# Performance work log

Measured on AMD Instinct MI355X. Metric: run time of the kernel, lower is better.

The kernel has to match this reference:

```python
import jax, jax.numpy as jnp
import numpy as np

EPS = 1e-12  # torch F.normalize eps


def _l2norm(x, axis):
    return x / jnp.maximum(jnp.linalg.norm(x, axis=axis, keepdims=True), EPS)


def setup_inputs() -> dict:
    key = jax.random.key(0)
    ks = jax.random.split(key, 8)
    B, N, D_in, H, K, D_out = 16, 1024, 1024, 512, 64, 1024
    return {
        "input_data": jax.random.normal(ks[0], (B, N, D_in), dtype=jnp.float32),
        "fc1_w": jax.random.normal(ks[1], (H, D_in), dtype=jnp.float32) * 0.02,
        "fc1_b": jax.random.normal(ks[2], (H,), dtype=jnp.float32) * 0.02,
        "conv_w": jax.random.normal(ks[3], (K, H), dtype=jnp.float32) * 0.1,
        "conv_b": jax.random.normal(ks[4], (K,), dtype=jnp.float32) * 0.1,
        "centroids": jax.random.normal(ks[5], (K, H), dtype=jnp.float32),
        "fc2_w": jax.random.normal(ks[6], (D_out, K * H), dtype=jnp.float32) * 0.01,
        "fc2_b": jax.random.normal(ks[7], (D_out,), dtype=jnp.float32) * 0.01,
    }


def reference(input_data, fc1_w, fc1_b, conv_w, conv_b, centroids, fc2_w, fc2_b):
    # fc1 + relu: [B, N, H]
    h = jax.nn.relu(jnp.einsum('bnd,hd->bnh', input_data, fc1_w) + fc1_b)
    # NetVLAD input layout: [B, H, N] (the (N,1) spatial dims collapse to N)
    x = jnp.swapaxes(h, 1, 2)
    # normalize descriptors across feature dim (F.normalize(x, p=2, dim=1))
    xn = _l2norm(x, axis=1)
    # 1x1-conv soft assignment -> softmax over clusters: [B, K, N]
    logits = jnp.einsum('kh,bhn->bkn', conv_w, xn) + conv_b[None, :, None]
    a = jax.nn.softmax(logits, axis=1)
    # vlad_{bkh} = sum_n a_{bkn} (xn_{bhn} - c_{kh})  (fused, no [B,K,H,N] tensor)
    vlad = jnp.einsum('bkn,bhn->bkh', a, xn) - a.sum(axis=-1)[:, :, None] * centroids[None]
    vlad = _l2norm(vlad, axis=2)              # intra-normalization
    vlad = vlad.reshape(vlad.shape[0], -1)    # [B, K*H]
    vlad = _l2norm(vlad, axis=1)              # global L2 norm
    # fc2 + relu: [B, out_dim]
    return jax.nn.relu(vlad @ fc2_w.T + fc2_b)
```

## Files before the change

### kernel.cpp

```cpp
#include <hip/hip_runtime.h>
#include <hip/hip_bf16.h>

typedef __bf16  bf16x8 __attribute__((ext_vector_type(8)));
typedef float   f32x4  __attribute__((ext_vector_type(4)));

#define DEV __device__ __forceinline__

DEV ushort f2b(float f){
  union { float f; unsigned u; } c; c.f = f;
  unsigned u = c.u;
  unsigned r = (u + 0x7FFFu + ((u >> 16) & 1u)) >> 16;
  return (ushort)r;
}
DEV float b2f(ushort h){
  union { unsigned u; float f; } c; c.u = ((unsigned)h) << 16;
  return c.f;
}
DEV void gload_lds16(const void* g, void* l){
  __builtin_amdgcn_global_load_lds(
      (const __attribute__((address_space(1))) void*)g,
      (__attribute__((address_space(3))) void*)l,
      16, 0, 0);
}
DEV bf16x8 cvt8(float4 a0, float4 a1){
  bf16x8 t;
  t[0]=(__bf16)a0.x; t[1]=(__bf16)a0.y; t[2]=(__bf16)a0.z; t[3]=(__bf16)a0.w;
  t[4]=(__bf16)a1.x; t[5]=(__bf16)a1.y; t[6]=(__bf16)a1.z; t[7]=(__bf16)a1.w;
  return t;
}

__global__ void prep(const float* __restrict__ W1, const float* __restrict__ CW,
                     const float* __restrict__ CB,
                     ushort* __restrict__ W1b, ushort* __restrict__ CWb,
                     float* __restrict__ CBp){
  int bid = blockIdx.x, tid = threadIdx.x;
  if(bid < 512){
    int i = bid * 256 + tid;
    float4 f = ((const float4*)W1)[i];
    ushort4 o; o.x = f2b(f.x); o.y = f2b(f.y); o.z = f2b(f.z); o.w = f2b(f.w);
    ((ushort4*)W1b)[i] = o;
  } else if(bid < 768){
    int i = (bid - 512) * 256 + tid;
    int r = i >> 9;
    CWb[i] = (r < 64) ? f2b(CW[i]) : (ushort)0;
  } else {
    if(tid < 128) CBp[tid] = (tid < 64) ? CB[tid] : 0.0f;
  }
}

__global__ __launch_bounds__(512) void fc1n(
    const float* __restrict__ A, const ushort* __restrict__ B,
    const float* __restrict__ bias, ushort* __restrict__ XN,
    ushort* __restrict__ XNT)
{
  const int K = 1024;
  __shared__ __align__(16) char smem[81920];
  __shared__ float ssq_p[4][64];
  __shared__ float scale_s[64];
  const int tid = threadIdx.x, lane = tid & 63, wid = tid >> 6;
  const int bm0 = blockIdx.x * 64;
  const int wr = (wid >> 2) * 32;
  const int wc = (wid & 3) * 128;
  const int wcol = wid & 3;

  const int srow = tid >> 3;
  const int sseg = tid & 7;
  const char* asrc = (const char*)A + (size_t)(bm0 + srow) * 4096
                     + (sseg ^ (srow & 7)) * 16;
  const int bslot = (tid & 3) ^ ((tid >> 3) & 3);
  const ushort* bg = B + (size_t)(tid >> 2) * K + bslot * 8;

  f32x4 acc[2][8];
  #pragma unroll
  for(int i = 0; i < 2; i++)
    #pragma unroll
    for(int j = 0; j < 8; j++) acc[i][j] = (f32x4){0.f, 0.f, 0.f, 0.f};

  const int arow = lane & 15;
  const int khalf = lane >> 4;

#define STAGE_F1N(buf, kb) do { \
    gload_lds16(asrc + (kb), smem + (buf) * 8192 + tid * 16); \
    const ushort* bs_ = bg + ((kb) >> 2); \
    char* bd_ = smem + 16384 + (buf) * 32768 + tid * 16; \
    gload_lds16(bs_,           bd_); \
    gload_lds16(bs_ + 128 * K, bd_ + 8192); \
    gload_lds16(bs_ + 256 * K, bd_ + 16384); \
    gload_lds16(bs_ + 384 * K, bd_ + 24576); \
  } while(0)

  STAGE_F1N(0, 0);
  __syncthreads();

  int cur = 0;
  for(int ks = 0; ks < 32; ++ks){
    if(ks + 1 < 32) STAGE_F1N(cur ^ 1, (ks + 1) * 128);
    bf16x8 af[2], bfr[8];
    #pragma unroll
    for(int mi = 0; mi < 2; mi++){
      int r = wr + mi * 16 + arow;
      const char* base = smem + cur * 8192 + r * 128;
      float4 a0 = *(const float4*)(base + (((khalf * 2)     ^ (r & 7)) * 16));
      float4 a1 = *(const float4*)(base + (((khalf * 2 + 1) ^ (r & 7)) * 16));
      af[mi] = cvt8(a0, a1);
    }
    #pragma unroll
    for(int ni = 0; ni < 8; ni++){
      int r = wc + ni * 16 + arow;
      bfr[ni] = *(const bf16x8*)(smem + 16384 + cur * 32768
                                 + r * 64 + ((khalf ^ ((r >> 1) & 3)) * 16));
    }
    #pragma unroll
    for(int mi = 0; mi < 2; mi++)
      #pragma unroll
      for(int ni = 0; ni < 8; ni++)
        acc[mi][ni] = __builtin_amdgcn_mfma_f32_16x16x32_bf16(af[mi], bfr[ni], acc[mi][ni], 0, 0, 0);
    __syncthreads();
    cur ^= 1;
  }
#undef STAGE_F1N

  float bv[8];
  #pragma unroll
  for(int ni = 0; ni < 8; ni++) bv[ni] = bias[wc + ni * 16 + (lane & 15)];
  float p[2][4];
  #pragma unroll
  for(int mi = 0; mi < 2; mi++)
    #pragma unroll
    for(int i = 0; i < 4; i++){
      float s = 0.f;
      #pragma unroll
      for(int ni = 0; ni < 8; ni++){
        float v = fmaxf(acc[mi][ni][i] + bv[ni], 0.f);
        acc[mi][ni][i] = v;
        s += v * v;
      }
      p[mi][i] = s;
    }
  #pragma unroll
  for(int o = 1; o < 16; o <<= 1)
    #pragma unroll
    for(int mi = 0; mi < 2; mi++)
      #pragma unroll
      for(int i = 0; i < 4; i++)
        p[mi][i] += __shfl_xor(p[mi][i], o, 64);
  if((lane & 15) == 0){
    int g = lane >> 4;
    #pragma unroll
    for(int mi = 0; mi < 2; mi++)
      #pragma unroll
      for(int i = 0; i < 4; i++)
        ssq_p[wcol][wr + mi * 16 + g * 4 + i] = p[mi][i];
  }
  __syncthreads();
  if(tid < 64){
    float s = ssq_p[0][tid] + ssq_p[1][tid] + ssq_p[2][tid] + ssq_p[3][tid];
    scale_s[tid] = 1.0f / fmaxf(sqrtf(s), 1e-12f);
  }
  __syncthreads();

  ushort* Tb = (ushort*)smem;
  #pragma unroll
  for(int mi = 0; mi < 2; mi++)
    #pragma unroll
    for(int i = 0; i < 4; i++){
      int rt = wr + mi * 16 + (lane >> 4) * 4 + i;
      float sc = scale_s[rt];
      #pragma unroll
      for(int ni = 0; ni < 8; ni++){
        int h = wc + ni * 16 + (lane & 15);
        ushort v = f2b(acc[mi][ni][i] * sc);
        XN[(size_t)(bm0 + rt) * 512 + h] = v;
        Tb[h * 66 + rt] = v;
      }
    }
  __syncthreads();
  {
    const int bb = bm0 >> 10, n0b = bm0 & 1023;
    const char* tb = (const char*)smem + tid * 132;
    unsigned tmp[32];
    #pragma unroll
    for(int j = 0; j < 32; j++) tmp[j] = *(const unsigned*)(tb + j * 4);
    ushort* dst = XNT + ((size_t)bb * 512 + tid) * 1024 + n0b;
    #pragma unroll
    for(int u = 0; u < 8; u++){
      uint4 w; w.x = tmp[u*4]; w.y = tmp[u*4+1]; w.z = tmp[u*4+2]; w.w = tmp[u*4+3];
      *(uint4*)(dst + u * 8) = w;
    }
  }
}

__global__ __launch_bounds__(256) void gemm_lgsm(
    const ushort* __restrict__ A, const ushort* __restrict__ B,
    const float* __restrict__ bias,
    ushort* __restrict__ AThi, ushort* __restrict__ ATlo)
{
  const int K = 512;
  __shared__ __align__(16) ushort As[2][64 * 32];
  __shared__ __align__(16) ushort Bs[2][128 * 32];
  __shared__ float as_[64][65];
  const int tid  = threadIdx.x;
  const int lane = tid & 63, wid = tid >> 6;
  const int bm0 = blockIdx.x * 64;
  const int wr = (wid >> 1) * 32, wc = (wid & 1) * 64;

  const int slot = (tid & 3) ^ ((tid >> 3) & 3);
  const ushort* ag = A + (size_t)(bm0 + (tid >> 2)) * K + slot * 8;
  const ushort* bg = B + (size_t)(tid >> 2) * K + slot * 8;

  f32x4 acc[2][4];
  #pragma unroll
  for(int i = 0; i < 2; i++)
    #pragma unroll
    for(int j = 0; j < 4; j++) acc[i][j] = (f32x4){0.f, 0.f, 0.f, 0.f};

  const int arow = lane & 15;
  const int khalf = lane >> 4;

  gload_lds16(ag,          &As[0][tid * 8]);
  gload_lds16(bg,          &Bs[0][tid * 8]);
  gload_lds16(bg + 64 * K, &Bs[0][2048 + tid * 8]);
  __syncthreads();

  int cur = 0;
  for(int ks = 0; ks < 16; ++ks){
    if(ks + 1 < 16){
      const ushort* agn = ag + (ks + 1) * 32;
      const ushort* bgn = bg + (ks + 1) * 32;
      gload_lds16(agn,          &As[cur ^ 1][tid * 8]);
      gload_lds16(bgn,          &Bs[cur ^ 1][tid * 8]);
      gload_lds16(bgn + 64 * K, &Bs[cur ^ 1][2048 + tid * 8]);
    }
    bf16x8 af[2], bfr[4];
    #pragma unroll
    for(int mi = 0; mi < 2; mi++){
      int r = wr + mi * 16 + arow;
      af[mi] = *(const bf16x8*)&As[cur][r * 32 + ((khalf ^ ((r >> 1) & 3)) * 8)];
    }
    #pragma unroll
    for(int ni = 0; ni < 4; ni++){
      int r = wc + ni * 16 + arow;
      bfr[ni] = *(const bf16x8*)&Bs[cur][r * 32 + ((khalf ^ ((r >> 1) & 3)) * 8)];
    }
    #pragma unroll
    for(int mi = 0; mi < 2; mi++)
      #pragma unroll
      for(int ni = 0; ni < 4; ni++)
        acc[mi][ni] = __builtin_amdgcn_mfma_f32_16x16x32_bf16(af[mi], bfr[ni], acc[mi][ni], 0, 0, 0);
    __syncthreads();
    cur ^= 1;
  }

  if((wid & 1) == 0){
    #pragma unroll
    for(int ni = 0; ni < 4; ni++){
      float bvv = bias[ni * 16 + (lane & 15)];
      #pragma unroll
      for(int mi = 0; mi < 2; mi++)
        #pragma unroll
        for(int i = 0; i < 4; i++) acc[mi][ni][i] += bvv;
    }
    #pragma unroll
    for(int mi = 0; mi < 2; mi++)
      #pragma unroll
      for(int i = 0; i < 4; i++){
        int row = wr + mi * 16 + (lane >> 4) * 4 + i;
        float m = fmaxf(fmaxf(acc[mi][0][i], acc[mi][1][i]),
                        fmaxf(acc[mi][2][i], acc[mi][3][i]));
        #pragma unroll
        for(int o = 1; o < 16; o <<= 1) m = fmaxf(m, __shfl_xor(m, o, 64));
        float e[4], s = 0.f;
        #pragma unroll
        for(int ni = 0; ni < 4; ni++){ e[ni] = __expf(acc[mi][ni][i] - m); s += e[ni]; }
        #pragma unroll
        for(int o = 1; o < 16; o <<= 1) s += __shfl_xor(s, o, 64);
        float inv = 1.0f / s;
        #pragma unroll
        for(int ni = 0; ni < 4; ni++)
          as_[row][ni * 16 + (lane & 15)] = e[ni] * inv;
      }
  }
  __syncthreads();

  const int b = bm0 >> 10, n0 = bm0 & 1023;
  const int nl = tid & 63, kq = tid >> 6;
  #pragma unroll
  for(int q = 0; q < 16; q++){
    int k = kq * 16 + q;
    float a = as_[nl][k];
    ushort hi = f2b(a);
    float lo = a - b2f(hi);
    size_t idx = ((size_t)b * 64 + k) * 1024 + n0 + nl;
    AThi[idx] = hi;
    ATlo[idx] = f2b(lo);
  }
}

__global__ __launch_bounds__(512) void vlad_mfma(
    const ushort* __restrict__ AThi, const ushort* __restrict__ ATlo,
    const ushort* __restrict__ XNT, const float* __restrict__ cent,
    ushort* __restrict__ vlb, float* __restrict__ ssq)
{
  __shared__ __align__(16) ushort Ah[2][16 * 32];
  __shared__ __align__(16) ushort Al[2][16 * 32];
  __shared__ __align__(16) ushort Xs[2][512 * 32];
  __shared__ float red[8][16];
  __shared__ float scale_s[16], ssqn_s[16];
  const int tid = threadIdx.x, lane = tid & 63, wid = tid >> 6;
  const int b = blockIdx.x, kg = blockIdx.y;
  const int k0 = kg * 16;
  const int hw = wid;
  const int arow = lane & 15, khalf = lane >> 4;

  const int xslot = (tid & 3) ^ ((tid >> 3) & 3);
  const ushort* xg = XNT + ((size_t)b * 512 + (tid >> 2)) * 1024 + xslot * 8;
  const int aslot = (lane & 3) ^ ((lane >> 3) & 3);
  const ushort* ahg = AThi + ((size_t)b * 64 + k0 + (lane >> 2)) * 1024 + aslot * 8;
  const ushort* alg = ATlo + ((size_t)b * 64 + k0 + (lane >> 2)) * 1024 + aslot * 8;

  f32x4 acc[4];
  #pragma unroll
  for(int i = 0; i < 4; i++) acc[i] = (f32x4){0.f, 0.f, 0.f, 0.f};
  f32x4 asum = (f32x4){0.f, 0.f, 0.f, 0.f};
  bf16x8 ones;
  #pragma unroll
  for(int j = 0; j < 8; j++) ones[j] = (__bf16)1.0f;

#define STAGE_VL(buf, n0v) do { \
    char* xd = (char*)&Xs[buf][0] + tid * 16; \
    gload_lds16(xg + (n0v),                xd); \
    gload_lds16(xg + (n0v) + 128 * 1024,   xd + 8192); \
    gload_lds16(xg + (n0v) + 256 * 1024,   xd + 16384); \
    gload_lds16(xg + (n0v) + 384 * 1024,   xd + 24576); \
    if(wid == 0)      gload_lds16(ahg + (n0v), (char*)&Ah[buf][0] + lane * 16); \
    else if(wid == 1) gload_lds16(alg + (n0v), (char*)&Al[buf][0] + lane * 16); \
  } while(0)

  STAGE_VL(0, 0);
  __syncthreads();

  int cur = 0;
  for(int ks = 0; ks < 32; ++ks){
    if(ks + 1 < 32) STAGE_VL(cur ^ 1, (ks + 1) * 32);
    bf16x8 ah, al, bfr[4];
    {
      int sl = khalf ^ ((arow >> 1) & 3);
      ah = *(const bf16x8*)&Ah[cur][arow * 32 + sl * 8];
      al = *(const bf16x8*)&Al[cur][arow * 32 + sl * 8];
    }
    #pragma unroll
    for(int ni = 0; ni < 4; ni++){
      int r = hw * 64 + ni * 16 + arow;
      bfr[ni] = *(const bf16x8*)&Xs[cur][r * 32 + ((khalf ^ ((r >> 1) & 3)) * 8)];
    }
    asum = __builtin_amdgcn_mfma_f32_16x16x32_bf16(ah, ones, asum, 0, 0, 0);
    asum = __builtin_amdgcn_mfma_f32_16x16x32_bf16(al, ones, asum, 0, 0, 0);
    #pragma unroll
    for(int ni = 0; ni < 4; ni++){
      acc[ni] = __builtin_amdgcn_mfma_f32_16x16x32_bf16(ah, bfr[ni], acc[ni], 0, 0, 0);
      acc[ni] = __builtin_amdgcn_mfma_f32_16x16x32_bf16(al, bfr[ni], acc[ni], 0, 0, 0);
    }
    __syncthreads();
    cur ^= 1;
  }
#undef STAGE_VL

  float vl[4][4];
  #pragma unroll
  for(int ni = 0; ni < 4; ni++)
    #pragma unroll
    for(int i = 0; i < 4; i++){
      int r_ = (lane >> 4) * 4 + i;
      int h = hw * 64 + ni * 16 + (lane & 15);
      vl[ni][i] = acc[ni][i] - asum[i] * cent[(size_t)(k0 + r_) * 512 + h];
    }
  float sq[4];
  #pragma unroll
  for(int i = 0; i < 4; i++){
    float s = 0.f;
    #pragma unroll
    for(int ni = 0; ni < 4; ni++) s += vl[ni][i] * vl[ni][i];
    sq[i] = s;
  }
  #pragma unroll
  for(int o = 1; o < 16; o <<= 1)
    #pragma unroll
    for(int i = 0; i < 4; i++) sq[i] += __shfl_xor(sq[i], o, 64);
  if((lane & 15) == 0){
    #pragma unroll
    for(int i = 0; i < 4; i++) red[hw][(lane >> 4) * 4 + i] = sq[i];
  }
  __syncthreads();
  if(tid < 16){
    float s = 0.f;
    #pragma unroll
    for(int w = 0; w < 8; w++) s += red[w][tid];
    float sc = 1.0f / fmaxf(sqrtf(s), 1e-12f);
    scale_s[tid] = sc;
    ssqn_s[tid] = s * sc * sc;
  }
  __syncthreads();
  if(tid < 4)
    ssq[b * 16 + kg * 4 + tid] = ssqn_s[tid * 4] + ssqn_s[tid * 4 + 1]
                               + ssqn_s[tid * 4 + 2] + ssqn_s[tid * 4 + 3];
  #pragma unroll
  for(int ni = 0; ni < 4; ni++)
    #pragma unroll
    for(int i = 0; i < 4; i++){
      int r_ = (lane >> 4) * 4 + i;
      int h = hw * 64 + ni * 16 + (lane & 15);
      vlb[(size_t)b * 32768 + (size_t)(k0 + r_) * 512 + h] = f2b(vl[ni][i] * scale_s[r_]);
    }
}

__global__ __launch_bounds__(256) void fc2_mfma(const float* __restrict__ W,
                                                const ushort* __restrict__ vlb,
                                                float* __restrict__ part){
  __shared__ __align__(16) float Bs[2][128 * 32];
  const int tid = threadIdx.x, lane = tid & 63, wid = tid >> 6;
  const int c0 = blockIdx.x * 128;
  const int kc = blockIdx.y;
  const size_t kbase = (size_t)kc * 256;

  const int srow = tid >> 3;
  const int seg  = tid & 7;
  f32x4 acc0 = (f32x4){0.f,0.f,0.f,0.f};
  f32x4 acc1 = (f32x4){0.f,0.f,0.f,0.f};

  const int arow = lane & 15;
  const int khalf = lane >> 4;
  const int cRow0 = wid * 32 + (lane & 15);
  const int cRow1 = cRow0 + 16;

  #pragma unroll
  for(int pass = 0; pass < 4; ++pass){
    int row = pass * 32 + srow;
    const char* src = (const char*)W + (size_t)(c0 + row) * 131072
                      + kbase * 4 + ((seg ^ (row & 7)) * 16);
    gload_lds16(src, (char*)&Bs[0][0] + row * 128 + seg * 16);
  }
  __syncthreads();

  int cur = 0;
  for(int ks = 0; ks < 8; ++ks){
    if(ks + 1 < 8){
      #pragma unroll
      for(int pass = 0; pass < 4; ++pass){
        int row = pass * 32 + srow;
        const char* src = (const char*)W + (size_t)(c0 + row) * 131072
                          + (kbase + (ks + 1) * 32) * 4 + ((seg ^ (row & 7)) * 16);
        gload_lds16(src, (char*)&Bs[cur ^ 1][0] + row * 128 + seg * 16);
      }
    }
    bf16x8 af = *(const bf16x8*)((const char*)vlb + (size_t)arow * 65536
                                 + (kbase + ks * 32 + khalf * 8) * 2);
    int t0 = khalf * 2;
    const char* bsc = (const char*)&Bs[cur][0];
    float4 b00 = *(const float4*)(bsc + cRow0 * 128 + ((t0     ^ (cRow0 & 7)) * 16));
    float4 b01 = *(const float4*)(bsc + cRow0 * 128 + (((t0+1) ^ (cRow0 & 7)) * 16));
    float4 b10 = *(const float4*)(bsc + cRow1 * 128 + ((t0     ^ (cRow1 & 7)) * 16));
    float4 b11 = *(const float4*)(bsc + cRow1 * 128 + (((t0+1) ^ (cRow1 & 7)) * 16));
    bf16x8 bf0 = cvt8(b00, b01);
    bf16x8 bf1 = cvt8(b10, b11);

    acc0 = __builtin_amdgcn_mfma_f32_16x16x32_bf16(af, bf0, acc0, 0, 0, 0);
    acc1 = __builtin_amdgcn_mfma_f32_16x16x32_bf16(af, bf1, acc1, 0, 0, 0);
    __syncthreads();
    cur ^= 1;
  }

  #pragma unroll
  for(int i = 0; i < 4; ++i){
    int b = (lane >> 4) * 4 + i;
    int d0 = c0 + wid * 32 + (lane & 15);
    part[((size_t)kc * 16 + b) * 1024 + d0]      = acc0[i];
    part[((size_t)kc * 16 + b) * 1024 + d0 + 16] = acc1[i];
  }
}

__global__ __launch_bounds__(256) void fin(const float* __restrict__ part, const float* __restrict__ ssq,
                                           const float* __restrict__ b2, float* __restrict__ out){
  __shared__ float red[4][64];
  int lane = threadIdx.x & 63, wq = threadIdx.x >> 6;
  int o = blockIdx.x * 64 + lane;
  int b = o >> 10, d = o & 1023;
  float s = 0;
  #pragma unroll
  for(int i = 0; i < 32; i++){
    int t = wq * 32 + i;
    s += part[((size_t)t * 16 + b) * 1024 + d];
  }
  red[wq][lane] = s;
  __syncthreads();
  if(wq == 0){
    float g = 0;
    #pragma unroll
    for(int kg = 0; kg < 16; kg++) g += ssq[b * 16 + kg];
    float gsv = 1.0f / fmaxf(sqrtf(g), 1e-12f);
    float tot = red[0][lane] + red[1][lane] + red[2][lane] + red[3][lane];
    out[o] = fmaxf(gsv * tot + b2[d], 0.0f);
  }
}

extern "C" void kernel_launch(void* const* d_in, const int* in_sizes, int n_in,
                              void* d_out, int out_size, void* d_ws, size_t ws_size,
                              hipStream_t stream){
  const float* X    = (const float*)d_in[0];
  const float* W1   = (const float*)d_in[1];
  const float* B1   = (const float*)d_in[2];
  const float* CW   = (const float*)d_in[3];
  const float* CB   = (const float*)d_in[4];
  const float* CENT = (const float*)d_in[5];
  const float* W2   = (const float*)d_in[6];
  const float* B2   = (const float*)d_in[7];
  float* out = (float*)d_out;
  char* ws = (char*)d_ws;

  ushort* W1b  = (ushort*)(ws + 0);
  ushort* CWb  = (ushort*)(ws + 1048576);
  float*  CBp  = (float*) (ws + 1179648);
  ushort* XN   = (ushort*)(ws + 1180160);
  ushort* XNT  = (ushort*)(ws + 17957376);
  ushort* AThi = (ushort*)(ws + 34734592);
  ushort* ATlo = (ushort*)(ws + 36831744);
  ushort* VLb  = (ushort*)(ws + 38928896);
  float*  SSQ  = (float*) (ws + 39977472);
  float*  PART = (float*) (ws + 39978496);

  prep<<<769, 256, 0, stream>>>(W1, CW, CB, W1b, CWb, CBp);
  fc1n<<<256, 512, 0, stream>>>(X, W1b, B1, XN, XNT);
  gemm_lgsm<<<256, 256, 0, stream>>>(XN, CWb, CBp, AThi, ATlo);
  vlad_mfma<<<dim3(16, 4), 512, 0, stream>>>(AThi, ATlo, XNT, CENT, VLb, SSQ);
  fc2_mfma<<<dim3(8, 128), 256, 0, stream>>>(W2, VLb, PART);
  fin<<<256, 256, 0, stream>>>(PART, SSQ, B2, out);
}
```

Measured before the change: 118.6 us.

## Fuse soft-assignment GEMM and softmax into fc1 normalize kernel

Folds the conv/soft-assignment GEMM and softmax into the fc1 kernel, keeping the normalized 64x512 tile in shared memory instead of writing the XN buffer and reading it back in a separate launch. The conv weights are pre-swizzled in prep and streamed into LDS per block. This removes one kernel launch and a 16 MB global round trip. In exchange, LDS per block grows to about 150 KB, which limits residency to one block per CU and adds serial work at the end of fc1.

After: 110.5 us. -6.9%, faster.

```diff
diff --git a/kernel.cpp b/kernel.cpp
--- a/kernel.cpp
+++ b/kernel.cpp
@@ -15,6 +15,16 @@
 DEV float b2f(ushort h){
   union { unsigned u; float f; } c; c.u = ((unsigned)h) << 16;
   return c.f;
+}
+DEV float wredsum(float v){
+  #pragma unroll
+  for(int o = 32; o > 0; o >>= 1) v += __shfl_xor(v, o, 64);
+  return v;
+}
+DEV float wredmax(float v){
+  #pragma unroll
+  for(int o = 32; o > 0; o >>= 1) v = fmaxf(v, __shfl_xor(v, o, 64));
+  return v;
 }
 DEV void gload_lds16(const void* g, void* l){
   __builtin_amdgcn_global_load_lds(
@@ -39,22 +49,24 @@
     float4 f = ((const float4*)W1)[i];
     ushort4 o; o.x = f2b(f.x); o.y = f2b(f.y); o.z = f2b(f.z); o.w = f2b(f.w);
     ((ushort4*)W1b)[i] = o;
-  } else if(bid < 768){
+  } else if(bid < 640){
     int i = (bid - 512) * 256 + tid;
-    int r = i >> 9;
-    CWb[i] = (r < 64) ? f2b(CW[i]) : (ushort)0;
+    int k = i >> 9, h = i & 511;
+    int seg = h >> 3, pos = h & 7;
+    CWb[(k << 9) + ((seg ^ (k & 7)) << 3) + pos] = f2b(CW[i]);
   } else {
     if(tid < 128) CBp[tid] = (tid < 64) ? CB[tid] : 0.0f;
   }
 }
 
-__global__ __launch_bounds__(512) void fc1n(
+__global__ __launch_bounds__(512) void fc1sm(
     const float* __restrict__ A, const ushort* __restrict__ B,
-    const float* __restrict__ bias, ushort* __restrict__ XN,
-    ushort* __restrict__ XNT)
+    const float* __restrict__ bias, const ushort* __restrict__ CWb,
+    const float* __restrict__ CBp, ushort* __restrict__ XNT,
+    ushort* __restrict__ AThi, ushort* __restrict__ ATlo)
 {
   const int K = 1024;
-  __shared__ __align__(16) char smem[81920];
+  __shared__ __align__(16) char smem[149504];
   __shared__ float ssq_p[4][64];
   __shared__ float scale_s[64];
   const int tid = threadIdx.x, lane = tid & 63, wid = tid >> 6;
@@ -159,7 +171,8 @@
   }
   __syncthreads();
 
-  ushort* Tb = (ushort*)smem;
+  ushort* Tb  = (ushort*)(smem + 81920);
+  ushort* xnm = (ushort*)smem;
   #pragma unroll
   for(int mi = 0; mi < 2; mi++)
     #pragma unroll
@@ -170,14 +183,15 @@
       for(int ni = 0; ni < 8; ni++){
         int h = wc + ni * 16 + (lane & 15);
         ushort v = f2b(acc[mi][ni][i] * sc);
-        XN[(size_t)(bm0 + rt) * 512 + h] = v;
         Tb[h * 66 + rt] = v;
+        xnm[rt * 520 + h] = v;
       }
     }
   __syncthreads();
+
+  const int bb = bm0 >> 10, n0b = bm0 & 1023;
   {
-    const int bb = bm0 >> 10, n0b = bm0 & 1023;
-    const char* tb = (const char*)smem + tid * 132;
+    const char* tb = (const char*)smem + 81920 + tid * 132;
     unsigned tmp[32];
     #pragma unroll
     for(int j = 0; j < 32; j++) tmp[j] = *(const unsigned*)(tb + j * 4);
@@ -188,111 +202,61 @@
       *(uint4*)(dst + u * 8) = w;
     }
   }
-}
-
-__global__ __launch_bounds__(256) void gemm_lgsm(
-    const ushort* __restrict__ A, const ushort* __restrict__ B,
-    const float* __restrict__ bias,
-    ushort* __restrict__ AThi, ushort* __restrict__ ATlo)
-{
-  const int K = 512;
-  __shared__ __align__(16) ushort As[2][64 * 32];
-  __shared__ __align__(16) ushort Bs[2][128 * 32];
-  __shared__ float as_[64][65];
-  const int tid  = threadIdx.x;
-  const int lane = tid & 63, wid = tid >> 6;
-  const int bm0 = blockIdx.x * 64;
-  const int wr = (wid >> 1) * 32, wc = (wid & 1) * 64;
-
-  const int slot = (tid & 3) ^ ((tid >> 3) & 3);
-  const ushort* ag = A + (size_t)(bm0 + (tid >> 2)) * K + slot * 8;
-  const ushort* bg = B + (size_t)(tid >> 2) * K + slot * 8;
-
-  f32x4 acc[2][4];
-  #pragma unroll
-  for(int i = 0; i < 2; i++)
-    #pragma unroll
-    for(int j = 0; j < 4; j++) acc[i][j] = (f32x4){0.f, 0.f, 0.f, 0.f};
-
-  const int arow = lane & 15;
-  const int khalf = lane >> 4;
-
-  gload_lds16(ag,          &As[0][tid * 8]);
-  gload_lds16(bg,          &Bs[0][tid * 8]);
-  gload_lds16(bg + 64 * K, &Bs[0][2048 + tid * 8]);
-  __syncthreads();
-
-  int cur = 0;
-  for(int ks = 0; ks < 16; ++ks){
-    if(ks + 1 < 16){
-      const ushort* agn = ag + (ks + 1) * 32;
-      const ushort* bgn = bg + (ks + 1) * 32;
-      gload_lds16(agn,          &As[cur ^ 1][tid * 8]);
-      gload_lds16(bgn,          &Bs[cur ^ 1][tid * 8]);
-      gload_lds16(bgn + 64 * K, &Bs[cur ^ 1][2048 + tid * 8]);
-    }
-    bf16x8 af[2], bfr[4];
-    #pragma unroll
-    for(int mi = 0; mi < 2; mi++){
-      int r = wr + mi * 16 + arow;
-      af[mi] = *(const bf16x8*)&As[cur][r * 32 + ((khalf ^ ((r >> 1) & 3)) * 8)];
-    }
-    #pragma unroll
-    for(int ni = 0; ni < 4; ni++){
-      int r = wc + ni * 16 + arow;
-      bfr[ni] = *(const bf16x8*)&Bs[cur][r * 32 + ((khalf ^ ((r >> 1) & 3)) * 8)];
-    }
+  __syncthreads();
+
+  char* CWs = smem + 66560;
+  #pragma unroll
+  for(int pp = 0; pp < 8; pp++)
+    gload_lds16((const char*)CWb + pp * 8192 + tid * 16, CWs + pp * 8192 + tid * 16);
+  __syncthreads();
+
+  float* as_ = (float*)(smem + 132096);
+  const int nt = (wid >> 2) * 32, kt = (wid & 3) * 16;
+  f32x4 acc2[2];
+  acc2[0] = (f32x4){0.f,0.f,0.f,0.f};
+  acc2[1] = (f32x4){0.f,0.f,0.f,0.f};
+  const int kr = kt + arow;
+  #pragma unroll
+  for(int s = 0; s < 16; ++s){
+    bf16x8 a0 = *(const bf16x8*)(smem + (size_t)(nt + arow) * 1040 + s * 64 + khalf * 16);
+    bf16x8 a1 = *(const bf16x8*)(smem + (size_t)(nt + 16 + arow) * 1040 + s * 64 + khalf * 16);
+    bf16x8 bw = *(const bf16x8*)(CWs + kr * 1024 + (((s * 4 + khalf) ^ (kr & 7)) * 16));
+    acc2[0] = __builtin_amdgcn_mfma_f32_16x16x32_bf16(a0, bw, acc2[0], 0, 0, 0);
+    acc2[1] = __builtin_amdgcn_mfma_f32_16x16x32_bf16(a1, bw, acc2[1], 0, 0, 0);
+  }
+  {
+    float bv2 = CBp[kt + (lane & 15)];
     #pragma unroll
     for(int mi = 0; mi < 2; mi++)
       #pragma unroll
-      for(int ni = 0; ni < 4; ni++)
-        acc[mi][ni] = __builtin_amdgcn_mfma_f32_16x16x32_bf16(af[mi], bfr[ni], acc[mi][ni], 0, 0, 0);
-    __syncthreads();
-    cur ^= 1;
-  }
-
-  if((wid & 1) == 0){
-    #pragma unroll
-    for(int ni = 0; ni < 4; ni++){
-      float bvv = bias[ni * 16 + (lane & 15)];
-      #pragma unroll
-      for(int mi = 0; mi < 2; mi++)
-        #pragma unroll
-        for(int i = 0; i < 4; i++) acc[mi][ni][i] += bvv;
-    }
-    #pragma unroll
-    for(int mi = 0; mi < 2; mi++)
-      #pragma unroll
-      for(int i = 0; i < 4; i++){
-        int row = wr + mi * 16 + (lane >> 4) * 4 + i;
-        float m = fmaxf(fmaxf(acc[mi][0][i], acc[mi][1][i]),
-                        fmaxf(acc[mi][2][i], acc[mi][3][i]));
-        #pragma unroll
-        for(int o = 1; o < 16; o <<= 1) m = fmaxf(m, __shfl_xor(m, o, 64));
-        float e[4], s = 0.f;
-        #pragma unroll
-        for(int ni = 0; ni < 4; ni++){ e[ni] = __expf(acc[mi][ni][i] - m); s += e[ni]; }
-        #pragma unroll
-        for(int o = 1; o < 16; o <<= 1) s += __shfl_xor(s, o, 64);
-        float inv = 1.0f / s;
-        #pragma unroll
-        for(int ni = 0; ni < 4; ni++)
-          as_[row][ni * 16 + (lane & 15)] = e[ni] * inv;
-      }
-  }
-  __syncthreads();
-
-  const int b = bm0 >> 10, n0 = bm0 & 1023;
-  const int nl = tid & 63, kq = tid >> 6;
-  #pragma unroll
-  for(int q = 0; q < 16; q++){
-    int k = kq * 16 + q;
-    float a = as_[nl][k];
-    ushort hi = f2b(a);
-    float lo = a - b2f(hi);
-    size_t idx = ((size_t)b * 64 + k) * 1024 + n0 + nl;
-    AThi[idx] = hi;
-    ATlo[idx] = f2b(lo);
+      for(int i = 0; i < 4; i++)
+        as_[(nt + mi * 16 + (lane >> 4) * 4 + i) * 65 + kt + (lane & 15)] = acc2[mi][i] + bv2;
+  }
+  __syncthreads();
+
+  #pragma unroll
+  for(int i = 0; i < 8; i++){
+    int rl = wid * 8 + i;
+    float l = as_[rl * 65 + lane];
+    float m = wredmax(l);
+    float e = __expf(l - m);
+    float s = wredsum(e);
+    as_[rl * 65 + lane] = e / s;
+  }
+  __syncthreads();
+
+  {
+    const int nl = tid & 63, kq = tid >> 6;
+    #pragma unroll
+    for(int q = 0; q < 8; q++){
+      int k = kq * 8 + q;
+      float a = as_[nl * 65 + k];
+      ushort hi = f2b(a);
+      float lo = a - b2f(hi);
+      size_t idx = ((size_t)bb * 64 + k) * 1024 + n0b + nl;
+      AThi[idx] = hi;
+      ATlo[idx] = f2b(lo);
+    }
   }
 }
 
@@ -518,18 +482,16 @@
 
   ushort* W1b  = (ushort*)(ws + 0);
   ushort* CWb  = (ushort*)(ws + 1048576);
-  float*  CBp  = (float*) (ws + 1179648);
-  ushort* XN   = (ushort*)(ws + 1180160);
-  ushort* XNT  = (ushort*)(ws + 17957376);
-  ushort* AThi = (ushort*)(ws + 34734592);
-  ushort* ATlo = (ushort*)(ws + 36831744);
-  ushort* VLb  = (ushort*)(ws + 38928896);
-  float*  SSQ  = (float*) (ws + 39977472);
-  float*  PART = (float*) (ws + 39978496);
-
-  prep<<<769, 256, 0, stream>>>(W1, CW, CB, W1b, CWb, CBp);
-  fc1n<<<256, 512, 0, stream>>>(X, W1b, B1, XN, XNT);
-  gemm_lgsm<<<256, 256, 0, stream>>>(XN, CWb, CBp, AThi, ATlo);
+  float*  CBp  = (float*) (ws + 1114112);
+  ushort* XNT  = (ushort*)(ws + 1114624);
+  ushort* AThi = (ushort*)(ws + 17891840);
+  ushort* ATlo = (ushort*)(ws + 19988992);
+  ushort* VLb  = (ushort*)(ws + 22086144);
+  float*  SSQ  = (float*) (ws + 23134720);
+  float*  PART = (float*) (ws + 23135744);
+
+  prep<<<641, 256, 0, stream>>>(W1, CW, CB, W1b, CWb, CBp);
+  fc1sm<<<256, 512, 0, stream>>>(X, W1b, B1, CWb, CBp, XNT, AThi, ATlo);
   vlad_mfma<<<dim3(16, 4), 512, 0, stream>>>(AThi, ATlo, XNT, CENT, VLb, SSQ);
   fc2_mfma<<<dim3(8, 128), 256, 0, stream>>>(W2, VLb, PART);
   fin<<<256, 256, 0, stream>>>(PART, SSQ, B2, out);
```
